# Kernel optimization log

Measured on AMD Instinct MI355X. Metric: run time of the kernel, lower is better.

## Reference

```python
import jax, jax.numpy as jnp
import numpy as np
from functools import partial

DIM = 256
HEADS = 8
RED = 4
HEAD_DIM = DIM // HEADS
SCALE = 1.0 / np.sqrt(HEAD_DIM).astype(np.float32)


def _conv(x, w, stride):
    # x: [B, C, H, W], w: [O, I, kh, kw] (OIHW), VALID padding
    return jax.lax.conv_general_dilated(
        x, w, window_strides=(stride, stride), padding='VALID',
        dimension_numbers=('NCHW', 'OIHW', 'NCHW'))


def setup_inputs() -> dict:
    key = jax.random.key(0)
    ks = jax.random.split(key, 5)
    B, H, W = 8, 64, 64
    x = jax.random.normal(ks[0], (B, DIM, H, W), dtype=jnp.float32)
    # conv weights, scaled like default kaiming-ish init
    wq = jax.random.normal(ks[1], (DIM, DIM, 1, 1), dtype=jnp.float32) / np.sqrt(DIM)
    wk = jax.random.normal(ks[2], (DIM, DIM, RED, RED), dtype=jnp.float32) / np.sqrt(DIM * RED * RED)
    wv = jax.random.normal(ks[3], (DIM, DIM, RED, RED), dtype=jnp.float32) / np.sqrt(DIM * RED * RED)
    wout = jax.random.normal(ks[4], (DIM, DIM, 1, 1), dtype=jnp.float32) / np.sqrt(DIM)
    return {"x": x, "wq": wq, "wk": wk, "wv": wv, "wout": wout}


def reference(x, wq, wk, wv, wout):
    B, C, H, W = x.shape
    q = _conv(x, wq, 1)            # [B, C, H, W]
    k = _conv(x, wk, RED)          # [B, C, H/r, W/r]
    v = _conv(x, wv, RED)          # [B, C, H/r, W/r]

    def split_heads(t):
        b, c, h, w = t.shape
        # b (n d) h w -> b n d (h w)
        return t.reshape(b, HEADS, HEAD_DIM, h * w)

    q, k, v = split_heads(q), split_heads(k), split_heads(v)
    # attn: [B, n, i, j], i = H*W, j = (H/r)*(W/r)
    attn = jnp.einsum('bndi,bndj->bnij', q, k) * SCALE
    attn = jax.nn.softmax(attn, axis=-1)
    out = jnp.einsum('bnij,bndj->bndi', attn, v)   # [B, n, d, H*W]
    out = out.reshape(B, C, H, W)                  # b (n d) h w
    return _conv(out, wout, 1)
```

## Files before the change

kernel.cpp:

```cpp
#include <hip/hip_runtime.h>
#include <hip/hip_bf16.h>


typedef __attribute__((ext_vector_type(8))) short s16x8;
typedef __attribute__((ext_vector_type(4))) short s16x4;
typedef __attribute__((ext_vector_type(4))) float f32x4;

#define MFMA16(a,b,c) __builtin_amdgcn_mfma_f32_16x16x32_bf16(a,b,c,0,0,0)

typedef const __attribute__((address_space(1))) void* gas1_t;
typedef __attribute__((address_space(3))) void* las3_t;

__device__ __forceinline__ unsigned short bfb(float f){
  __hip_bfloat16 h = __float2bfloat16(f);
  return __builtin_bit_cast(unsigned short, h);
}

__device__ __forceinline__ void async16(void* l, const void* g){
  __builtin_amdgcn_global_load_lds((gas1_t)g, (las3_t)l, 16, 0, 0);
}

__global__ __launch_bounds__(256) void k_cvt_w(const float* __restrict__ wq,
                                               const float* __restrict__ wk,
                                               const float* __restrict__ wv,
                                               const float* __restrict__ wo,
                                               unsigned short* __restrict__ dst){
  int c = blockIdx.x*256 + threadIdx.x;
  int e = c*4;
  const float* s; int off;
  if (e < 65536)        { s = wq; off = e; }
  else if (e < 1114112) { s = wk; off = e - 65536; }
  else if (e < 2162688) { s = wv; off = e - 1114112; }
  else                  { s = wo; off = e - 2162688; }
  float4 f = *(const float4*)(s + off);
  s16x4 o; o[0]=(short)bfb(f.x); o[1]=(short)bfb(f.y); o[2]=(short)bfb(f.z); o[3]=(short)bfb(f.w);
  *(s16x4*)(dst + e) = o;
}

__global__ __launch_bounds__(256) void k_cvt_x(const float* __restrict__ x,
                                               unsigned short* __restrict__ xT,
                                               unsigned short* __restrict__ xcolT){
  __shared__ __align__(16) unsigned short lx[32*4*72];
  const int cc = blockIdx.x, hc = blockIdx.y, b = blockIdx.z;
  const int ci0 = cc*32, h0 = hc*4;
  const int t = threadIdx.x;
  #pragma unroll
  for (int s=0; s<8; ++s){
    int c = s*256 + t;
    int ci = c>>6, rem = c&63, kh = rem>>4, wq = rem&15;
    float4 f = *(const float4*)(x + ((size_t)((b*256+ci0+ci)*64 + h0+kh)*64 + wq*4));
    s16x4 o; o[0]=(short)bfb(f.x); o[1]=(short)bfb(f.y); o[2]=(short)bfb(f.z); o[3]=(short)bfb(f.w);
    *(s16x4*)(&lx[(ci*4+kh)*72 + wq*4]) = o;
  }
  __syncthreads();
  {
    int kh = t>>6, w = t&63;
    size_t p = (size_t)(h0+kh)*64 + w;
    unsigned short* dst = xT + ((size_t)b*4096 + p)*256 + ci0;
    s16x8 o[4];
    #pragma unroll
    for (int c2=0;c2<32;c2++) o[c2>>3][c2&7] = (short)lx[(c2*4+kh)*72 + w];
    #pragma unroll
    for (int q2=0;q2<4;q2++) *(s16x8*)(dst + q2*8) = o[q2];
  }
  {
    int w2 = t&15, u = t>>4;
    int pr = hc*16 + w2;
    unsigned short* dst = xcolT + ((size_t)b*256 + pr)*4096 + (ci0 + u*2)*16;
    s16x8 o[4];
    #pragma unroll
    for (int c2=0;c2<2;c2++)
      #pragma unroll
      for (int kh=0;kh<4;kh++)
        #pragma unroll
        for (int kw=0;kw<4;kw++)
          o[c2*2 + (kh>>1)][(kh&1)*4 + kw] = (short)lx[((u*2+c2)*4+kh)*72 + w2*4 + kw];
    #pragma unroll
    for (int q2=0;q2<4;q2++) *(s16x8*)(dst + q2*8) = o[q2];
  }
}

template<int MODE>
__device__ __forceinline__ void gemm_core(const unsigned short* __restrict__ A,
                                          const unsigned short* __restrict__ B,
                                          void* __restrict__ O,
                                          int ldA, int ldB, int ldO,
                                          int m0, int n0, int kOfs, int nK){
  __shared__ __align__(16) unsigned short As[128*32];
  __shared__ __align__(16) unsigned short Bs[128*32];
  const int t = threadIdx.x;
  const int lane = t & 63, wvi = t >> 6;
  const int wm = (wvi>>1)*64, wn = (wvi&1)*64;
  const int g = lane>>4, l15 = lane&15;
  f32x4 acc[4][4];
  #pragma unroll
  for (int i=0;i<4;i++)
    #pragma unroll
    for (int j=0;j<4;j++) acc[i][j] = f32x4{0.f,0.f,0.f,0.f};

  for (int kt=0; kt<nK; ++kt){
    const int k0 = kOfs + kt*32;
    __syncthreads();
    #pragma unroll
    for (int s=0;s<2;s++){
      int chunk = s*256 + t;
      int row = chunk>>2, kq = chunk&3;
      async16(&As[chunk*8], A + (size_t)(m0+row)*ldA + k0 + kq*8);
    }
    #pragma unroll
    for (int s=0;s<2;s++){
      int chunk = s*256 + t;
      int row = chunk>>2, kq = chunk&3;
      async16(&Bs[chunk*8], B + (size_t)(n0+row)*ldB + k0 + kq*8);
    }
    __syncthreads();
    s16x8 af[4], bv[4];
    #pragma unroll
    for (int i=0;i<4;i++) af[i] = *(const s16x8*)(&As[(wm + i*16 + l15)*32 + g*8]);
    #pragma unroll
    for (int j=0;j<4;j++) bv[j] = *(const s16x8*)(&Bs[(wn + j*16 + l15)*32 + g*8]);
    #pragma unroll
    for (int i=0;i<4;i++)
      #pragma unroll
      for (int j=0;j<4;j++)
        acc[i][j] = MFMA16(af[i], bv[j], acc[i][j]);
  }

  if (MODE == 0){
    unsigned short* Ou = (unsigned short*)O;
    #pragma unroll
    for (int i=0;i<4;i++)
      #pragma unroll
      for (int j=0;j<4;j++){
        int mm = m0 + wm + i*16 + g*4;
        int nn = n0 + wn + j*16 + l15;
        #pragma unroll
        for (int r=0;r<4;r++) Ou[(size_t)(mm+r)*ldO + nn] = bfb(acc[i][j][r]);
      }
  } else if (MODE == 1){
    float* Of = (float*)O;
    #pragma unroll
    for (int i=0;i<4;i++)
      #pragma unroll
      for (int j=0;j<4;j++){
        int mm = m0 + wm + i*16 + g*4;
        int nn = n0 + wn + j*16 + l15;
        *(f32x4*)(Of + (size_t)nn*ldO + mm) = acc[i][j];
      }
  } else {
    float* Of = (float*)O;
    #pragma unroll
    for (int i=0;i<4;i++)
      #pragma unroll
      for (int j=0;j<4;j++){
        int mm = m0 + wm + i*16 + g*4;
        int nn = n0 + wn + j*16 + l15;
        #pragma unroll
        for (int r=0;r<4;r++) Of[(size_t)(mm+r)*ldO + nn] = acc[i][j][r];
      }
  }
}

__global__ __launch_bounds__(256,2) void k_gemm_q(const unsigned short* __restrict__ xT,
                                                  const unsigned short* __restrict__ wqb,
                                                  unsigned short* __restrict__ Qt){
  int b = blockIdx.z;
  gemm_core<0>(xT + (size_t)b*1048576, wqb, Qt + (size_t)b*1048576,
               256, 256, 256, blockIdx.y*128, blockIdx.x*128, 0, 8);
}

__global__ __launch_bounds__(256,2) void k_gemm_kv(const unsigned short* __restrict__ wkb,
                                                   const unsigned short* __restrict__ wvb,
                                                   const unsigned short* __restrict__ xcol,
                                                   float* __restrict__ part){
  int zz = blockIdx.z; int s = zz&3, w = (zz>>2)&1, b = zz>>3;
  const unsigned short* A = w ? wvb : wkb;
  gemm_core<2>(A, xcol + (size_t)b*1048576,
               part + ((size_t)((w*8+b)*4 + s))*65536,
               4096, 4096, 256, blockIdx.y*128, blockIdx.x*128, s*1024, 32);
}

__global__ __launch_bounds__(256,2) void k_gemm_out(const unsigned short* __restrict__ attnT,
                                                    const unsigned short* __restrict__ wob,
                                                    float* __restrict__ out){
  int b = blockIdx.z;
  gemm_core<1>(attnT + (size_t)b*1048576, wob, out + (size_t)b*1048576,
               256, 256, 4096, blockIdx.y*128, blockIdx.x*128, 0, 8);
}

__global__ __launch_bounds__(256) void k_reduce_kv(const float* __restrict__ part,
                                                   unsigned short* __restrict__ Kt,
                                                   unsigned short* __restrict__ Vv){
  unsigned idx = blockIdx.x*256 + threadIdx.x;
  int j = idx & 255, co = (idx>>8)&255, bb = (idx>>16)&7, w = idx>>19;
  const float* p = part + (size_t)((w*8+bb)*4)*65536 + co*256 + j;
  float s = p[0] + p[65536] + p[131072] + p[196608];
  if (w==0) Kt[((size_t)bb*256 + j)*256 + co] = bfb(s);
  else      Vv[((size_t)bb*256 + co)*256 + j] = bfb(s);
}

__global__ __launch_bounds__(256,4) void k_attn(const unsigned short* __restrict__ Qt,
                                                const unsigned short* __restrict__ Kt,
                                                const unsigned short* __restrict__ Vv,
                                                unsigned short* __restrict__ attnT){
  __shared__ __align__(16) unsigned short P[4*16*256];
  const int itile = blockIdx.x, n = blockIdx.y, b = blockIdx.z;
  const int t = threadIdx.x, wv = t>>6, lane = t&63, g = lane>>4, l15 = lane&15;
  const int i0 = itile*64 + wv*16;
  const f32x4 zero = {0.f,0.f,0.f,0.f};
  const float kexp = 0.17677669529663687f * 1.4426950408889634f;

  const s16x8 qf = *(const s16x8*)(Qt + ((size_t)(b*4096 + i0 + l15))*256 + n*32 + g*8);

  char* pb = (char*)&P[wv*16*256];
  const int swz = (l15&7)<<4;
  float lsum = 0.f;

  #pragma unroll
  for (int jt=0;jt<16;jt++){
    s16x8 kf = *(const s16x8*)(Kt + ((size_t)(b*256 + jt*16 + l15))*256 + n*32 + g*8);
    f32x4 s = MFMA16(kf, qf, zero);
    float e0 = exp2f(s[0]*kexp), e1 = exp2f(s[1]*kexp);
    float e2 = exp2f(s[2]*kexp), e3 = exp2f(s[3]*kexp);
    lsum += (e0+e1)+(e2+e3);
    s16x4 w4; w4[0]=(short)bfb(e0); w4[1]=(short)bfb(e1); w4[2]=(short)bfb(e2); w4[3]=(short)bfb(e3);
    int byte = (l15<<9) + ((jt*16 + g*4)<<1);
    *(s16x4*)(pb + (byte ^ swz)) = w4;
  }
  lsum += __shfl_xor(lsum, 16);
  lsum += __shfl_xor(lsum, 32);
  float rcp_r[4];
  #pragma unroll
  for (int r=0;r<4;r++) rcp_r[r] = __builtin_amdgcn_rcpf(__shfl(lsum, g*4+r));

  f32x4 oacc[2] = {zero, zero};
  #pragma unroll
  for (int kt=0;kt<8;kt++){
    int byte = (l15<<9) + ((kt*32 + g*8)<<1);
    s16x8 pa = *(const s16x8*)(pb + (byte ^ swz));
    #pragma unroll
    for (int dt=0;dt<2;dt++){
      s16x8 vf = *(const s16x8*)(Vv + ((size_t)(b*256 + n*32 + dt*16 + l15))*256 + kt*32 + g*8);
      oacc[dt] = MFMA16(pa, vf, oacc[dt]);
    }
  }
  #pragma unroll
  for (int dt=0;dt<2;dt++)
    #pragma unroll
    for (int r=0;r<4;r++)
      attnT[((size_t)(b*4096 + i0 + g*4 + r))*256 + n*32 + dt*16 + l15] = bfb(oacc[dt][r]*rcp_r[r]);
}

extern "C" void kernel_launch(void* const* d_in, const int* in_sizes, int n_in,
                              void* d_out, int out_size, void* d_ws, size_t ws_size,
                              hipStream_t stream){
  (void)in_sizes; (void)n_in; (void)out_size; (void)ws_size;
  const float* x    = (const float*)d_in[0];
  const float* wq   = (const float*)d_in[1];
  const float* wk   = (const float*)d_in[2];
  const float* wv   = (const float*)d_in[3];
  const float* wout = (const float*)d_in[4];
  char* ws = (char*)d_ws;

  unsigned short* wb    = (unsigned short*)(ws + 0);
  unsigned short* xT    = (unsigned short*)(ws + 4456448);
  unsigned short* xcol  = (unsigned short*)(ws + 21233664);
  unsigned short* Qt    = (unsigned short*)(ws + 38010880);
  unsigned short* Kt    = (unsigned short*)(ws + 54788096);
  unsigned short* Vv    = (unsigned short*)(ws + 55836672);
  float*          part  = (float*)(ws + 4456448);
  unsigned short* attnT = (unsigned short*)(ws + 21233664);
  float* out = (float*)d_out;

  unsigned short* wqb = wb;
  unsigned short* wkb = wb + 65536;
  unsigned short* wvb = wb + 1114112;
  unsigned short* wob = wb + 2162688;

  k_cvt_w   <<<2176,            256, 0, stream>>>(wq, wk, wv, wout, wb);
  k_cvt_x   <<<dim3(8,16,8),    256, 0, stream>>>(x, xT, xcol);
  k_gemm_q  <<<dim3(2,32,8),    256, 0, stream>>>(xT, wqb, Qt);
  k_gemm_kv <<<dim3(2,2,64),    256, 0, stream>>>(wkb, wvb, xcol, part);
  k_reduce_kv<<<4096,           256, 0, stream>>>(part, Kt, Vv);
  k_attn    <<<dim3(64,8,8),    256, 0, stream>>>(Qt, Kt, Vv, attnT);
  k_gemm_out<<<dim3(2,32,8),    256, 0, stream>>>(attnT, wob, out);
}
```

Baseline: 218.1 us.

## Stage K/V in LDS with 32x32 MFMA attention and deeper split-K for KV GEMM

Result: faster. 183.0 us (-16.1%).

```diff
diff --git a/kernel.cpp b/kernel.cpp
--- a/kernel.cpp
+++ b/kernel.cpp
@@ -5,8 +5,10 @@
 typedef __attribute__((ext_vector_type(8))) short s16x8;
 typedef __attribute__((ext_vector_type(4))) short s16x4;
 typedef __attribute__((ext_vector_type(4))) float f32x4;
+typedef __attribute__((ext_vector_type(16))) float f32x16;
 
 #define MFMA16(a,b,c) __builtin_amdgcn_mfma_f32_16x16x32_bf16(a,b,c,0,0,0)
+#define MFMA32(a,b,c) __builtin_amdgcn_mfma_f32_32x32x16_bf16(a,b,c,0,0,0)
 
 typedef const __attribute__((address_space(1))) void* gas1_t;
 typedef __attribute__((address_space(3))) void* las3_t;
@@ -172,12 +174,12 @@
 __global__ __launch_bounds__(256,2) void k_gemm_kv(const unsigned short* __restrict__ wkb,
                                                    const unsigned short* __restrict__ wvb,
                                                    const unsigned short* __restrict__ xcol,
-                                                   float* __restrict__ part){
-  int zz = blockIdx.z; int s = zz&3, w = (zz>>2)&1, b = zz>>3;
+                                                   float* __restrict__ part, int S){
+  int zz = blockIdx.z; int s = zz % S; int rest = zz / S; int w = rest & 1, b = rest >> 1;
   const unsigned short* A = w ? wvb : wkb;
   gemm_core<2>(A, xcol + (size_t)b*1048576,
-               part + ((size_t)((w*8+b)*4 + s))*65536,
-               4096, 4096, 256, blockIdx.y*128, blockIdx.x*128, s*1024, 32);
+               part + ((size_t)((w*8+b)*S + s))*65536,
+               4096, 4096, 256, blockIdx.y*128, blockIdx.x*128, s*(4096/S), 128/S);
 }
 
 __global__ __launch_bounds__(256,2) void k_gemm_out(const unsigned short* __restrict__ attnT,
@@ -190,71 +192,94 @@
 
 __global__ __launch_bounds__(256) void k_reduce_kv(const float* __restrict__ part,
                                                    unsigned short* __restrict__ Kt,
-                                                   unsigned short* __restrict__ Vv){
+                                                   unsigned short* __restrict__ Vv, int S){
   unsigned idx = blockIdx.x*256 + threadIdx.x;
   int j = idx & 255, co = (idx>>8)&255, bb = (idx>>16)&7, w = idx>>19;
-  const float* p = part + (size_t)((w*8+bb)*4)*65536 + co*256 + j;
-  float s = p[0] + p[65536] + p[131072] + p[196608];
-  if (w==0) Kt[((size_t)bb*256 + j)*256 + co] = bfb(s);
-  else      Vv[((size_t)bb*256 + co)*256 + j] = bfb(s);
-}
-
-__global__ __launch_bounds__(256,4) void k_attn(const unsigned short* __restrict__ Qt,
+  const float* p = part + (size_t)((w*8+bb)*S)*65536 + co*256 + j;
+  float sum = 0.f;
+  for (int s2=0;s2<S;s2++) sum += p[(size_t)s2*65536];
+  if (w==0) Kt[((size_t)bb*256 + j)*256 + co] = bfb(sum);
+  else      Vv[((size_t)bb*256 + co)*256 + j] = bfb(sum);
+}
+
+__global__ __launch_bounds__(256,3) void k_attn(const unsigned short* __restrict__ Qt,
                                                 const unsigned short* __restrict__ Kt,
                                                 const unsigned short* __restrict__ Vv,
                                                 unsigned short* __restrict__ attnT){
-  __shared__ __align__(16) unsigned short P[4*16*256];
-  const int itile = blockIdx.x, n = blockIdx.y, b = blockIdx.z;
-  const int t = threadIdx.x, wv = t>>6, lane = t&63, g = lane>>4, l15 = lane&15;
-  const int i0 = itile*64 + wv*16;
-  const f32x4 zero = {0.f,0.f,0.f,0.f};
+  __shared__ __align__(16) char smem[43008];
+  const int xb = blockIdx.x, n = blockIdx.y, b = blockIdx.z;
+  const int t = threadIdx.x, wv = t>>6, lane = t&63, hi = lane>>5, l31 = lane&31;
+  char* Ks = smem;
+  char* Vs = smem + 16384;
+  char* Pb = smem + 32768 + wv*2560;
   const float kexp = 0.17677669529663687f * 1.4426950408889634f;
 
-  const s16x8 qf = *(const s16x8*)(Qt + ((size_t)(b*4096 + i0 + l15))*256 + n*32 + g*8);
-
-  char* pb = (char*)&P[wv*16*256];
-  const int swz = (l15&7)<<4;
-  float lsum = 0.f;
-
-  #pragma unroll
-  for (int jt=0;jt<16;jt++){
-    s16x8 kf = *(const s16x8*)(Kt + ((size_t)(b*256 + jt*16 + l15))*256 + n*32 + g*8);
-    f32x4 s = MFMA16(kf, qf, zero);
-    float e0 = exp2f(s[0]*kexp), e1 = exp2f(s[1]*kexp);
-    float e2 = exp2f(s[2]*kexp), e3 = exp2f(s[3]*kexp);
-    lsum += (e0+e1)+(e2+e3);
-    s16x4 w4; w4[0]=(short)bfb(e0); w4[1]=(short)bfb(e1); w4[2]=(short)bfb(e2); w4[3]=(short)bfb(e3);
-    int byte = (l15<<9) + ((jt*16 + g*4)<<1);
-    *(s16x4*)(pb + (byte ^ swz)) = w4;
-  }
-  lsum += __shfl_xor(lsum, 16);
-  lsum += __shfl_xor(lsum, 32);
-  float rcp_r[4];
-  #pragma unroll
-  for (int r=0;r<4;r++) rcp_r[r] = __builtin_amdgcn_rcpf(__shfl(lsum, g*4+r));
-
-  f32x4 oacc[2] = {zero, zero};
-  #pragma unroll
-  for (int kt=0;kt<8;kt++){
-    int byte = (l15<<9) + ((kt*32 + g*8)<<1);
-    s16x8 pa = *(const s16x8*)(pb + (byte ^ swz));
-    #pragma unroll
-    for (int dt=0;dt<2;dt++){
-      s16x8 vf = *(const s16x8*)(Vv + ((size_t)(b*256 + n*32 + dt*16 + l15))*256 + kt*32 + g*8);
-      oacc[dt] = MFMA16(pa, vf, oacc[dt]);
+  #pragma unroll
+  for (int s=0;s<4;s++){
+    int flat = s*256 + t;
+    int j = flat>>2, cc = flat&3;
+    int gc = cc ^ ((j>>1)&3);
+    async16(Ks + flat*16, Kt + ((size_t)b<<16) + j*256 + n*32 + gc*8);
+  }
+  #pragma unroll
+  for (int s=0;s<4;s++){
+    int flat = s*256 + t;
+    int d = flat>>5, c = flat&31;
+    int gc = c ^ (d&7);
+    async16(Vs + flat*16, Vv + ((size_t)b<<16) + (size_t)(n*32+d)*256 + gc*8);
+  }
+  __syncthreads();
+
+  const int swj = (l31>>1)&3;
+  const int swv = l31&7;
+
+  #pragma unroll
+  for (int it=0; it<2; ++it){
+    const int i0 = xb*256 + it*128 + wv*32;
+    const s16x8 q0 = *(const s16x8*)(Qt + ((size_t)(b*4096 + i0 + l31))*256 + n*32 + hi*8);
+    const s16x8 q1 = *(const s16x8*)(Qt + ((size_t)(b*4096 + i0 + l31))*256 + n*32 + 16 + hi*8);
+    f32x16 oacc = {};
+    float lsum = 0.f;
+
+    #pragma unroll
+    for (int jb=0;jb<8;jb++){
+      const int krow = (jb*32 + l31)*64;
+      s16x8 kf0 = *(const s16x8*)(Ks + krow + (((0+hi) ^ swj)<<4));
+      s16x8 kf1 = *(const s16x8*)(Ks + krow + (((2+hi) ^ swj)<<4));
+      f32x16 sS = MFMA32(kf0, q0, (f32x16){});
+      sS = MFMA32(kf1, q1, sS);
+      float e[16];
+      #pragma unroll
+      for (int r=0;r<16;r++){ e[r] = exp2f(sS[r]*kexp); lsum += e[r]; }
+      #pragma unroll
+      for (int q4=0;q4<4;q4++){
+        s16x4 w4; w4[0]=(short)bfb(e[4*q4+0]); w4[1]=(short)bfb(e[4*q4+1]);
+                  w4[2]=(short)bfb(e[4*q4+2]); w4[3]=(short)bfb(e[4*q4+3]);
+        *(s16x4*)(Pb + l31*80 + q4*16 + hi*8) = w4;
+      }
+      #pragma unroll
+      for (int ks=0;ks<2;ks++){
+        s16x8 pa = *(const s16x8*)(Pb + l31*80 + ks*32 + hi*16);
+        s16x8 vf = *(const s16x8*)(Vs + l31*512 + (((jb*4 + ks*2 + hi) ^ swv)<<4));
+        oacc = MFMA32(pa, vf, oacc);
+      }
     }
-  }
-  #pragma unroll
-  for (int dt=0;dt<2;dt++)
-    #pragma unroll
-    for (int r=0;r<4;r++)
-      attnT[((size_t)(b*4096 + i0 + g*4 + r))*256 + n*32 + dt*16 + l15] = bfb(oacc[dt][r]*rcp_r[r]);
+    lsum += __shfl_xor(lsum, 32);
+    float rcp = __builtin_amdgcn_rcpf(lsum);
+    const int hi4 = hi*4;
+    #pragma unroll
+    for (int r=0;r<16;r++){
+      int i_r = (r&3) + 8*(r>>2) + hi4;
+      float sc = __shfl(rcp, i_r);
+      attnT[((size_t)(b*4096 + i0 + i_r))*256 + n*32 + l31] = bfb(oacc[r]*sc);
+    }
+  }
 }
 
 extern "C" void kernel_launch(void* const* d_in, const int* in_sizes, int n_in,
                               void* d_out, int out_size, void* d_ws, size_t ws_size,
                               hipStream_t stream){
-  (void)in_sizes; (void)n_in; (void)out_size; (void)ws_size;
+  (void)in_sizes; (void)n_in; (void)out_size;
   const float* x    = (const float*)d_in[0];
   const float* wq   = (const float*)d_in[1];
   const float* wk   = (const float*)d_in[2];
@@ -268,9 +293,14 @@
   unsigned short* Qt    = (unsigned short*)(ws + 38010880);
   unsigned short* Kt    = (unsigned short*)(ws + 54788096);
   unsigned short* Vv    = (unsigned short*)(ws + 55836672);
-  float*          part  = (float*)(ws + 4456448);
   unsigned short* attnT = (unsigned short*)(ws + 21233664);
   float* out = (float*)d_out;
+
+  const size_t part8_off = 56885248ull;
+  const size_t part8_end = part8_off + 2ull*8*8*65536*4;
+  int S; float* part;
+  if (ws_size >= part8_end) { S = 8; part = (float*)(ws + part8_off); }
+  else                      { S = 4; part = (float*)(ws + 4456448); }
 
   unsigned short* wqb = wb;
   unsigned short* wkb = wb + 65536;
@@ -280,8 +310,8 @@
   k_cvt_w   <<<2176,            256, 0, stream>>>(wq, wk, wv, wout, wb);
   k_cvt_x   <<<dim3(8,16,8),    256, 0, stream>>>(x, xT, xcol);
   k_gemm_q  <<<dim3(2,32,8),    256, 0, stream>>>(xT, wqb, Qt);
-  k_gemm_kv <<<dim3(2,2,64),    256, 0, stream>>>(wkb, wvb, xcol, part);
-  k_reduce_kv<<<4096,           256, 0, stream>>>(part, Kt, Vv);
-  k_attn    <<<dim3(64,8,8),    256, 0, stream>>>(Qt, Kt, Vv, attnT);
+  k_gemm_kv <<<dim3(2,2,16*S),  256, 0, stream>>>(wkb, wvb, xcol, part, S);
+  k_reduce_kv<<<4096,           256, 0, stream>>>(part, Kt, Vv, S);
+  k_attn    <<<dim3(16,8,8),    256, 0, stream>>>(Qt, Kt, Vv, attnT);
   k_gemm_out<<<dim3(2,32,8),    256, 0, stream>>>(attnT, wob, out);
 }
```
